# Kernel tuning notes

Measured on AMD Instinct MI355X. Metric: run time of the kernel, lower is better.

The kernel has to match this reference:

```python
import jax, jax.numpy as jnp
import numpy as np

DIM = 768; HEADS = 12; HEAD_DIM = 64; WIN = 14; AC = 192; R = 32; S = 1.0
SCALE = HEAD_DIM ** -0.5
EPS = 1e-5  # torch nn.LayerNorm default


def _ln(x, w, b):
    mu = x.mean(-1, keepdims=True)
    var = ((x - mu) ** 2).mean(-1, keepdims=True)
    return (x - mu) * jax.lax.rsqrt(var + EPS) * w + b


def _rel(rel_pos, n):
    # q_size == k_size == n, rel_pos has 2n-1 rows -> no interpolation branch
    coords = jnp.arange(n)[:, None] - jnp.arange(n)[None, :] + (n - 1)
    return rel_pos[coords]  # [n, n, HEAD_DIM]


def _window_partition(x, ws):
    B, H, W, C = x.shape
    ph = (ws - H % ws) % ws; pw = (ws - W % ws) % ws
    x = jnp.pad(x, ((0, 0), (0, ph), (0, pw), (0, 0)))
    Hp, Wp = H + ph, W + pw
    x = x.reshape(B, Hp // ws, ws, Wp // ws, ws, C).transpose(0, 1, 3, 2, 4, 5)
    return x.reshape(-1, ws, ws, C), (Hp, Wp)


def _window_unpartition(win, ws, pad_hw, hw):
    Hp, Wp = pad_hw; H, W = hw
    B = win.shape[0] // (Hp * Wp // ws // ws)
    x = win.reshape(B, Hp // ws, Wp // ws, ws, ws, -1).transpose(0, 1, 3, 2, 4, 5)
    x = x.reshape(B, Hp, Wp, -1)
    return x[:, :H, :W, :]


def _attention(xw, qkv_W, qkv_b, facu_W, facv_W, qfac_W, vfac_W, rel_h, rel_w, proj_W, proj_b):
    Bw, h, w, _ = xw.shape
    N = h * w
    qkv = xw @ qkv_W.T + qkv_b                     # [Bw, h, w, 3*DIM]
    fu = xw @ facu_W.T                              # FacTu; dropout = identity (eval)
    new_q = (fu @ qfac_W.T) @ facv_W.T              # q_FacTs -> FacTv
    new_v = (fu @ vfac_W.T) @ facv_W.T              # v_FacTs -> FacTv
    qkv = qkv.at[..., :DIM].add(new_q * S)
    qkv = qkv.at[..., 2 * DIM:].add(new_v * S)
    qkv = qkv.reshape(Bw, N, 3, HEADS, HEAD_DIM).transpose(2, 0, 3, 1, 4)
    qkv = qkv.reshape(3, Bw * HEADS, N, HEAD_DIM)
    q, k, v = qkv[0], qkv[1], qkv[2]
    attn = (q * SCALE) @ k.transpose(0, 2, 1)       # [Bw*HEADS, N, N]
    Rh = _rel(rel_h, h); Rw = _rel(rel_w, w)
    r_q = q.reshape(-1, h, w, HEAD_DIM)
    dh = jnp.einsum('bhwc,hkc->bhwk', r_q, Rh)
    dw = jnp.einsum('bhwc,wkc->bhwk', r_q, Rw)
    attn = (attn.reshape(-1, h, w, h, w) + dh[:, :, :, :, None] + dw[:, :, :, None, :]).reshape(-1, N, N)
    attn = jax.nn.softmax(attn, axis=-1)
    out = (attn @ v).reshape(Bw, HEADS, h, w, HEAD_DIM).transpose(0, 2, 3, 1, 4).reshape(Bw, h, w, DIM)
    return out @ proj_W.T + proj_b


def _adapter(x, d_size, nw, nb, dW, db, cW, cb, uW, ub):
    b, h, w, _ = x.shape
    y = _ln(x, nw, nb)
    y = y @ dW.T + db                               # [b, h, w, AC]
    y = y.reshape(b // d_size, d_size, h, w, AC).transpose(0, 4, 1, 2, 3)  # NCDHW
    y = jax.lax.conv_general_dilated(y, cW, (1, 1, 1), 'SAME',
                                     dimension_numbers=('NCDHW', 'OIDHW', 'NCDHW'))
    y = y + cb[None, :, None, None, None]
    y = y.transpose(0, 2, 3, 4, 1).reshape(b, h, w, AC)
    y = jax.nn.gelu(y, approximate=False)
    return x + (y @ uW.T + ub)


def reference(x, an1_w, an1_b, ad1_W, ad1_b, ac1_W, ac1_b, au1_W, au1_b,
              n1_w, n1_b, qkv_W, qkv_b, facu_W, facv_W, qfac_W, vfac_W,
              rel_h, rel_w, proj_W, proj_b,
              an2_w, an2_b, ad2_W, ad2_b, ac2_W, ac2_b, au2_W, au2_b,
              n2_w, n2_b, mlp_W1, mlp_b1, mlp_W2, mlp_b2, d_size):
    x = _adapter(x, d_size, an1_w, an1_b, ad1_W, ad1_b, ac1_W, ac1_b, au1_W, au1_b)
    shortcut = x
    y = _ln(x, n1_w, n1_b)
    H, W = y.shape[1], y.shape[2]
    y, pad_hw = _window_partition(y, WIN)
    y = _attention(y, qkv_W, qkv_b, facu_W, facv_W, qfac_W, vfac_W, rel_h, rel_w, proj_W, proj_b)
    y = _window_unpartition(y, WIN, pad_hw, (H, W))
    x = shortcut + y
    x = _adapter(x, d_size, an2_w, an2_b, ad2_W, ad2_b, ac2_W, ac2_b, au2_W, au2_b)
    h = _ln(x, n2_w, n2_b)
    h = jax.nn.gelu(h @ mlp_W1.T + mlp_b1, approximate=False)
    return x + (h @ mlp_W2.T + mlp_b2)


def setup_inputs() -> dict:
    key = jax.random.key(0)
    ks = iter(jax.random.split(key, 64))
    def rn(shape, scale=0.02):
        return jax.random.normal(next(ks), shape, dtype=jnp.float32) * scale
    B, D, HW = 1, 5, 64
    inp = {'x': jax.random.normal(next(ks), (B * D, HW, HW, DIM), dtype=jnp.float32)}
    for p in ('1', '2'):
        inp[f'an{p}_w'] = jnp.ones((DIM,), jnp.float32)
        inp[f'an{p}_b'] = jnp.zeros((DIM,), jnp.float32)
        inp[f'ad{p}_W'] = rn((AC, DIM)); inp[f'ad{p}_b'] = jnp.zeros((AC,), jnp.float32)
        inp[f'ac{p}_W'] = rn((AC, AC, 3, 3, 3)); inp[f'ac{p}_b'] = jnp.zeros((AC,), jnp.float32)
        inp[f'au{p}_W'] = rn((DIM, AC)); inp[f'au{p}_b'] = jnp.zeros((DIM,), jnp.float32)
    inp['n1_w'] = jnp.ones((DIM,), jnp.float32); inp['n1_b'] = jnp.zeros((DIM,), jnp.float32)
    inp['qkv_W'] = rn((3 * DIM, DIM)); inp['qkv_b'] = jnp.zeros((3 * DIM,), jnp.float32)
    inp['facu_W'] = rn((R, DIM)); inp['facv_W'] = rn((DIM, R))
    inp['qfac_W'] = rn((R, R)); inp['vfac_W'] = rn((R, R))
    inp['rel_h'] = rn((2 * WIN - 1, HEAD_DIM)); inp['rel_w'] = rn((2 * WIN - 1, HEAD_DIM))
    inp['proj_W'] = rn((DIM, DIM)); inp['proj_b'] = jnp.zeros((DIM,), jnp.float32)
    inp['n2_w'] = jnp.ones((DIM,), jnp.float32); inp['n2_b'] = jnp.zeros((DIM,), jnp.float32)
    inp['mlp_W1'] = rn((4 * DIM, DIM)); inp['mlp_b1'] = jnp.zeros((4 * DIM,), jnp.float32)
    inp['mlp_W2'] = rn((DIM, 4 * DIM)); inp['mlp_b2'] = jnp.zeros((DIM,), jnp.float32)
    inp['d_size'] = D
    return inp
```

## Files before the change

### kernel.cpp

```cpp
#include <hip/hip_runtime.h>

typedef unsigned short u16;
typedef __bf16 v8bf __attribute__((ext_vector_type(8)));
typedef unsigned short v8u __attribute__((ext_vector_type(8)));
typedef unsigned short v4u __attribute__((ext_vector_type(4)));
typedef float f32x4 __attribute__((ext_vector_type(4)));
typedef float v8f __attribute__((ext_vector_type(8)));

static constexpr int DIMC = 768;
static constexpr int HEADS = 12;
static constexpr int WINS  = 14;
static constexpr int ACCH  = 192;
static constexpr int NTOK  = 196;
static constexpr int MW    = 24500;
static constexpr int MWP   = 24576;
static constexpr int MS    = 20480;

__device__ __forceinline__ float bf2f(u16 u) {
  union { unsigned int i; float f; } x; x.i = ((unsigned int)u) << 16; return x.f;
}
__device__ __forceinline__ u16 f2bf(float f) {
  union { float f; unsigned int i; } x; x.f = f;
  unsigned int r = x.i + 0x7fffu + ((x.i >> 16) & 1u);
  return (u16)(r >> 16);
}
__device__ __forceinline__ float gelu_f(float x) {
  float y = 0.79788456080286536f * (x + 0.044715f * x * x * x);
  y = fminf(fmaxf(y, -15.f), 15.f);
  const float e = __expf(2.f * y);
  const float th = 1.f - 2.f * __builtin_amdgcn_rcpf(e + 1.f);
  return 0.5f * x * (1.f + th);
}
__device__ __forceinline__ void cp16(const u16* g, u16* l) {
  __builtin_amdgcn_global_load_lds(
      (const __attribute__((address_space(1))) unsigned int*)(const void*)g,
      (__attribute__((address_space(3))) unsigned int*)(void*)l, 16, 0, 0);
}

__global__ void k_zero16(u16* p, int n) {
  int i = blockIdx.x * 256 + threadIdx.x;
  if (i < n) p[i] = 0;
}
__global__ void k_compute_U(const float* __restrict__ facu, const float* __restrict__ qfac,
                            const float* __restrict__ vfac, float* __restrict__ Uq,
                            float* __restrict__ Uv) {
  int idx = blockIdx.x * 256 + threadIdx.x;
  if (idx >= 2 * 768 * 32) return;
  const int which = idx / (768 * 32);
  const int rem = idx - which * 768 * 32;
  const int k = rem >> 5, b = rem & 31;
  const float* fac = which ? vfac : qfac;
  float s = 0.f;
  for (int a = 0; a < 32; ++a) s += facu[a * 768 + k] * fac[b * 32 + a];
  (which ? Uv : Uq)[rem] = s;
}
__global__ void k_build_wcomb(const float* __restrict__ qkvW, const float* __restrict__ Uq,
                              const float* __restrict__ Uv, const float* __restrict__ facv,
                              u16* __restrict__ Wc) {
  int idx = blockIdx.x * 256 + threadIdx.x;
  if (idx >= 2304 * 768) return;
  const int n = idx / 768, k = idx - n * 768;
  float v = qkvW[idx];
  if (n < 768) {
    float s = 0.f;
    for (int b = 0; b < 32; ++b) s += Uq[k * 32 + b] * facv[n * 32 + b];
    v += s;
  } else if (n >= 1536) {
    const int nn = n - 1536;
    float s = 0.f;
    for (int b = 0; b < 32; ++b) s += Uv[k * 32 + b] * facv[nn * 32 + b];
    v += s;
  }
  Wc[idx] = f2bf(v);
}
__global__ void k_cast_pad(const float* __restrict__ src, u16* __restrict__ dst,
                           int rows, int cols, int rowsPad) {
  int idx = blockIdx.x * 256 + threadIdx.x;
  const int base = idx * 4;
  if (base >= rowsPad * cols) return;
  const int r = base / cols;
  v4u o;
  if (r < rows) {
    const float4 v = *(const float4*)(src + base);
    o[0] = f2bf(v.x); o[1] = f2bf(v.y); o[2] = f2bf(v.z); o[3] = f2bf(v.w);
  } else {
    o[0] = o[1] = o[2] = o[3] = 0;
  }
  *(v4u*)(dst + base) = o;
}
__global__ void k_conv_repack(const float* __restrict__ src, u16* __restrict__ dst) {
  int idx = blockIdx.x * 256 + threadIdx.x;
  const int base = idx * 4;
  if (base >= 256 * 5184) return;
  const int co = base / 5184;
  const int rem = base - co * 5184;
  const int tap = rem / 192, ci = rem - tap * 192;
  v4u o;
  if (co < 192) {
    const float* sp = src + co * 5184 + ci * 27 + tap;
#pragma unroll
    for (int e = 0; e < 4; ++e) o[e] = f2bf(sp[e * 27]);
  } else {
    o[0] = o[1] = o[2] = o[3] = 0;
  }
  *(v4u*)(dst + base) = o;
}

template<bool WINDOWED>
__global__ __launch_bounds__(256)
void ln_k(const float* __restrict__ X, const float* __restrict__ w,
          const float* __restrict__ b, u16* __restrict__ out) {
  const int r = (int)blockIdx.x;
  const int t = (int)threadIdx.x;
  int src = r;
  bool zero = false;
  if (WINDOWED) {
    if (r >= MW) zero = true;
    else {
      const int win = r / NTOK, tk = r - win * NTOK;
      const int img = win / 25, wrem = win - img * 25, wy = wrem / 5, wx = wrem - wy * 5;
      const int ty = tk / WINS, tx = tk - ty * WINS;
      const int y = wy * WINS + ty, x = wx * WINS + tx;
      if (y >= 64 || x >= 64) zero = true;
      else src = (img << 12) + (y << 6) + x;
    }
  }
  u16* orow = out + (size_t)r * DIMC;
  if (zero) {
    for (int c = t; c < DIMC; c += 256) orow[c] = 0;
    return;
  }
  const float* xr = X + (size_t)src * DIMC;
  const float v0 = xr[t], v1 = xr[t + 256], v2 = xr[t + 512];
  float s = v0 + v1 + v2, ss = v0 * v0 + v1 * v1 + v2 * v2;
#pragma unroll
  for (int o = 32; o > 0; o >>= 1) { s += __shfl_xor(s, o, 64); ss += __shfl_xor(ss, o, 64); }
  __shared__ float red[8];
  const int wave = t >> 6, lane = t & 63;
  if (lane == 0) { red[wave] = s; red[4 + wave] = ss; }
  __syncthreads();
  s = red[0] + red[1] + red[2] + red[3];
  ss = red[4] + red[5] + red[6] + red[7];
  const float mean = s * (1.0f / 768.0f);
  const float var = ss * (1.0f / 768.0f) - mean * mean;
  const float rstd = rsqrtf(var + 1e-5f);
  orow[t]       = f2bf((v0 - mean) * rstd * w[t]       + b[t]);
  orow[t + 256] = f2bf((v1 - mean) * rstd * w[t + 256] + b[t + 256]);
  orow[t + 512] = f2bf((v2 - mean) * rstd * w[t + 512] + b[t + 512]);
}

template<int EPI, bool CONV>
__global__ __launch_bounds__(256)
void gemm_bt(const u16* __restrict__ A, const u16* __restrict__ B,
             const float* __restrict__ bias, const float* __restrict__ resid,
             float* __restrict__ outF, u16* __restrict__ outB,
             int M, int N, int K, const u16* __restrict__ zrow, int GN) {
  __shared__ u16 smem[2 * 128 * 64];
  u16* At = smem;
  u16* Bt = smem + 128 * 64;
  const int gx = (int)gridDim.x;
  const int nwg = gx * (int)gridDim.y;
  const int lin = (int)blockIdx.y * gx + (int)blockIdx.x;
  const int csz = nwg >> 3;
  const int xcd = lin & 7;
  const int c = lin >> 3;
  const int bmc = csz / gx;
  const int gsz = bmc * GN;
  const int grp = c / gsz, rr = c - grp * gsz;
  const int bn = grp * GN + (rr % GN);
  const int bm = xcd * bmc + (rr / GN);
  const int t = (int)threadIdx.x;
  const int wave = t >> 6, lane = t & 63;
  const int wm = wave >> 1, wn = wave & 1;
  const int lrow = lane >> 3;
  const int c16s = (lane & 7) ^ lrow;
  const int li = lane & 15, lq = lane >> 4;

  f32x4 acc[4][4];
  const f32x4 vzero = {0.f, 0.f, 0.f, 0.f};
#pragma unroll
  for (int a = 0; a < 4; ++a)
#pragma unroll
    for (int b = 0; b < 4; ++b) acc[a][b] = vzero;

  const int nk = K >> 6;
  for (int kt = 0; kt < nk; ++kt) {
    int cD = 0, cY = 0, cX = 0, cblk = 0;
    if (CONV) {
      const int tap = kt / 3;
      cblk = (kt - tap * 3) << 6;
      const int kd = tap / 9, r9 = tap - kd * 9, ky = r9 / 3;
      cD = kd - 1; cY = ky - 1; cX = (r9 - ky * 3) - 1;
    }
#pragma unroll
    for (int i = 0; i < 4; ++i) {
      const int r0 = i * 32 + wave * 8;
      const int grow = bm * 128 + r0 + lrow;
      const u16* src;
      if (CONV) {
        const int d = (grow >> 12) + cD, y = ((grow >> 6) & 63) + cY, x = (grow & 63) + cX;
        if ((unsigned)d < 5u && (unsigned)y < 64u && (unsigned)x < 64u)
          src = A + (size_t)((d << 12) + (y << 6) + x) * ACCH + cblk + c16s * 8;
        else
          src = zrow + c16s * 8;
      } else {
        src = A + (size_t)grow * K + (kt << 6) + c16s * 8;
      }
      cp16(src, &At[r0 * 64]);
    }
#pragma unroll
    for (int i = 0; i < 4; ++i) {
      const int r0 = i * 32 + wave * 8;
      const int grow = bn * 128 + r0 + lrow;
      cp16(B + (size_t)grow * K + (kt << 6) + c16s * 8, &Bt[r0 * 64]);
    }
    __syncthreads();
#pragma unroll
    for (int kk = 0; kk < 2; ++kk) {
      v8bf af[4], bg[4];
#pragma unroll
      for (int mf = 0; mf < 4; ++mf) {
        const int row = wm * 64 + mf * 16 + li;
        const int c16 = (kk * 4 + lq) ^ (li & 7);
        af[mf] = *(const v8bf*)&At[row * 64 + c16 * 8];
      }
#pragma unroll
      for (int nf = 0; nf < 4; ++nf) {
        const int row = wn * 64 + nf * 16 + li;
        const int c16 = (kk * 4 + lq) ^ (li & 7);
        bg[nf] = *(const v8bf*)&Bt[row * 64 + c16 * 8];
      }
#pragma unroll
      for (int mf = 0; mf < 4; ++mf)
#pragma unroll
        for (int nf = 0; nf < 4; ++nf)
          acc[mf][nf] = __builtin_amdgcn_mfma_f32_16x16x32_bf16(af[mf], bg[nf], acc[mf][nf], 0, 0, 0);
    }
    __syncthreads();
  }

  if (EPI == 1 || EPI == 2 || EPI == 4) {
    u16* Ct = smem;
#pragma unroll
    for (int mf = 0; mf < 4; ++mf)
#pragma unroll
      for (int nf = 0; nf < 4; ++nf)
#pragma unroll
        for (int r = 0; r < 4; ++r) {
          const int row = wm * 64 + mf * 16 + lq * 4 + r;
          const int col = wn * 64 + nf * 16 + li;
          float v = acc[mf][nf][r] + bias[bn * 128 + col];
          if (EPI == 2) v = gelu_f(v);
          Ct[row * 128 + (col ^ ((row & 7) << 3))] = f2bf(v);
        }
    __syncthreads();
#pragma unroll
    for (int it = 0; it < 8; ++it) {
      const int row = it * 16 + (t >> 4);
      const int seg = t & 15;
      const int gr = bm * 128 + row;
      const int col8 = bn * 128 + seg * 8;
      if (gr < M && col8 < N) {
        v8u val = *(const v8u*)&Ct[row * 128 + ((seg ^ (row & 7)) * 8)];
        if (EPI == 4) {
          const int sec = col8 / 768;
          const int hm = col8 - sec * 768;
          const int hd = hm >> 6, dd = hm & 63;
          const int win = gr / 196, tk = gr - win * 196;
          *(v8u*)(outB + (size_t)(((win * HEADS + hd) * 3 + sec) * NTOK + tk) * 64 + dd) = val;
        } else {
          *(v8u*)(outB + (size_t)gr * N + col8) = val;
        }
      }
    }
  } else {
    float* Cf = (float*)smem;
#pragma unroll
    for (int h2 = 0; h2 < 2; ++h2) {
      if (h2) __syncthreads();
      if (wm == h2) {
#pragma unroll
        for (int mf = 0; mf < 4; ++mf)
#pragma unroll
          for (int nf = 0; nf < 4; ++nf)
#pragma unroll
            for (int r = 0; r < 4; ++r) {
              const int row = mf * 16 + lq * 4 + r;
              const int col = wn * 64 + nf * 16 + li;
              const float v = acc[mf][nf][r] + bias[bn * 128 + col];
              Cf[row * 128 + (col ^ (((row >> 2) & 3) << 3))] = v;
            }
      }
      __syncthreads();
#pragma unroll
      for (int it = 0; it < 4; ++it) {
        const int row = it * 16 + (t >> 4);
        const int seg = t & 15;
        const int gr = bm * 128 + h2 * 64 + row;
        const int col8 = bn * 128 + seg * 8;
        if (gr < M && col8 < N) {
          v8f val = *(const v8f*)&Cf[row * 128 + ((seg ^ ((row >> 2) & 3)) * 8)];
          if (EPI == 3) {
            const float* rp = resid + (size_t)gr * N + col8;
#pragma unroll
            for (int e = 0; e < 8; ++e) val[e] += rp[e];
            *(v8f*)(outF + (size_t)gr * N + col8) = val;
          } else {
            const int win = gr / 196, tk = gr - win * 196;
            const int img = win / 25, wrem = win - img * 25, wy = wrem / 5, wx = wrem - wy * 5;
            const int ty = tk / WINS, tx = tk - ty * WINS;
            const int y = wy * WINS + ty, x = wx * WINS + tx;
            if (y < 64 && x < 64) {
              const size_t o = (size_t)((img << 12) + (y << 6) + x) * DIMC + col8;
              const float* rp = resid + o;
#pragma unroll
              for (int e = 0; e < 8; ++e) val[e] += rp[e];
              *(v8f*)(outF + o) = val;
            }
          }
        }
      }
    }
  }
}

__global__ __launch_bounds__(512, 2)
void attn_k(const u16* __restrict__ qkvR, const float* __restrict__ relh,
            const float* __restrict__ relw, u16* __restrict__ out) {
  const int blk = (int)blockIdx.x;
  const int win = blk / HEADS, h = blk - win * HEADS;
  const int t = (int)threadIdx.x, w = t >> 6, lane = t & 63;
  const int li = lane & 15, g = lane >> 4;
  const int nmf = (w < 6) ? 2 : (w == 6 ? 1 : 0);

  __shared__ u16 Kt[64 * 64];
  __shared__ u16 Vt[64 * 64];
  __shared__ u16 Pb[8 * 32 * 32];
  __shared__ u16 dhwT[28 * 268];

  const u16* Qb = qkvR + (size_t)(win * HEADS + h) * 3 * NTOK * 64;
  const u16* Kb = Qb + NTOK * 64;
  const u16* Vb = Kb + NTOK * 64;

  v8bf qf[2][2];
#pragma unroll
  for (int mf = 0; mf < 2; ++mf) {
    const int row = min(32 * w + mf * 16 + li, NTOK - 1);
#pragma unroll
    for (int ks = 0; ks < 2; ++ks)
      qf[mf][ks] = *(const v8bf*)(Qb + (size_t)row * 64 + ks * 32 + g * 8);
  }

  u16* relb = Pb;
  for (int idx = t; idx < 2 * 32 * 64; idx += 512) {
    const int which = idx >> 11, rem = idx & 2047, r = rem >> 6, c = rem & 63;
    const float v = (r < 27) ? (which ? relw[r * 64 + c] : relh[r * 64 + c]) : 0.f;
    relb[which * 2048 + r * 64 + (((c >> 3) ^ (r & 7)) * 8) + (c & 7)] = f2bf(v);
  }
  __syncthreads();

  {
    f32x4 dacc[2][2], eacc[2][2];
    const f32x4 vz = {0.f, 0.f, 0.f, 0.f};
#pragma unroll
    for (int mf = 0; mf < 2; ++mf)
#pragma unroll
      for (int nf = 0; nf < 2; ++nf) { dacc[mf][nf] = vz; eacc[mf][nf] = vz; }
#pragma unroll
    for (int ks = 0; ks < 2; ++ks) {
#pragma unroll
      for (int nf = 0; nf < 2; ++nf) {
        const int row = nf * 16 + li;
        const int off = row * 64 + (((ks * 4 + g) ^ (li & 7)) * 8);
        v8bf bh = *(const v8bf*)&relb[off];
        v8bf bw = *(const v8bf*)&relb[2048 + off];
#pragma unroll
        for (int mf = 0; mf < 2; ++mf) if (mf < nmf) {
          dacc[mf][nf] = __builtin_amdgcn_mfma_f32_16x16x32_bf16(qf[mf][ks], bh, dacc[mf][nf], 0, 0, 0);
          eacc[mf][nf] = __builtin_amdgcn_mfma_f32_16x16x32_bf16(qf[mf][ks], bw, eacc[mf][nf], 0, 0, 0);
        }
      }
    }
#pragma unroll
    for (int mf = 0; mf < 2; ++mf) if (mf < nmf)
#pragma unroll
      for (int nf = 0; nf < 2; ++nf)
#pragma unroll
        for (int r = 0; r < 4; ++r) {
          const int i = 32 * w + mf * 16 + 4 * g + r;
          if (i < 196) {
            const int c = nf * 16 + li;
            const int ih = (i * 2341) >> 15, iw = i - ih * 14;
            const int jh = ih + 13 - c;
            if ((unsigned)jh < 14u) dhwT[jh * 268 + i] = f2bf(dacc[mf][nf][r]);
            const int jw = iw + 13 - c;
            if ((unsigned)jw < 14u) dhwT[(14 + jw) * 268 + i] = f2bf(eacc[mf][nf][r]);
          }
        }
  }
  __syncthreads();

  f32x4 oacc[2][4];
  const f32x4 vz = {0.f, 0.f, 0.f, 0.f};
#pragma unroll
  for (int a = 0; a < 2; ++a)
#pragma unroll
    for (int b = 0; b < 4; ++b) oacc[a][b] = vz;
  float mrun[8], lrun[8];
#pragma unroll
  for (int a = 0; a < 8; ++a) { mrun[a] = -1e30f; lrun[a] = 0.f; }

  u16* Pw = Pb + w * 1024;
  const int jv = t & 63;
  const int dv = w * 8;

  for (int jt = 0; jt < 4; ++jt) {
    const int j0 = jt * 64;
    const int njf = (jt < 3) ? 4 : 1;
    const int nhalf = (jt < 3) ? 2 : 1;

    {
      const int rbase = w * 8;
      const int row = rbase + (lane >> 3);
      const int jg = min(j0 + row, NTOK - 1);
      const int cbs = (lane & 7) ^ (row & 7);
      cp16(Kb + (size_t)jg * 64 + cbs * 8, &Kt[rbase * 64]);
    }
    __builtin_amdgcn_sched_barrier(0);
    const int jgv = min(j0 + jv, NTOK - 1);
    v8u vg = *(const v8u*)(Vb + (size_t)jgv * 64 + dv);
    __builtin_amdgcn_sched_barrier(0);
    asm volatile("s_waitcnt vmcnt(1)" ::: "memory");
    __builtin_amdgcn_sched_barrier(0);
    __builtin_amdgcn_s_barrier();
    __builtin_amdgcn_sched_barrier(0);

    f32x4 sacc[2][4];
#pragma unroll
    for (int a = 0; a < 2; ++a)
#pragma unroll
      for (int b = 0; b < 4; ++b) sacc[a][b] = vz;
    if (nmf > 0) {
#pragma unroll
      for (int ks = 0; ks < 2; ++ks) {
#pragma unroll
        for (int jf = 0; jf < 4; ++jf) if (jf < njf) {
          const int row = jf * 16 + li;
          v8bf kb = *(const v8bf*)&Kt[row * 64 + (((ks * 4 + g) ^ (li & 7)) * 8)];
#pragma unroll
          for (int mf = 0; mf < 2; ++mf) if (mf < nmf)
            sacc[mf][jf] = __builtin_amdgcn_mfma_f32_16x16x32_bf16(qf[mf][ks], kb, sacc[mf][jf], 0, 0, 0);
        }
      }
    }

    asm volatile("s_waitcnt vmcnt(0)" ::: "memory");
    __builtin_amdgcn_sched_barrier(0);
#pragma unroll
    for (int e = 0; e < 8; ++e) {
      const int da = dv + e;
      Vt[da * 64 + (((jv >> 3) ^ (da & 7)) * 8) + (jv & 7)] = vg[e];
    }

#pragma unroll
    for (int jf = 0; jf < 4; ++jf) if (jf < njf) {
      const int j = j0 + jf * 16 + li;
      const bool jok = j < 196;
      int jh = (j * 2341) >> 15;
      const int jw = j - jh * 14;
      if (jh > 13) jh = 13;
#pragma unroll
      for (int mf = 0; mf < 2; ++mf) if (mf < nmf) {
        const int i0 = 32 * w + mf * 16 + 4 * g;
        v4u hv = *(const v4u*)&dhwT[jh * 268 + i0];
        v4u wv = *(const v4u*)&dhwT[(14 + jw) * 268 + i0];
#pragma unroll
        for (int r = 0; r < 4; ++r) {
          float v;
          if (jok && (i0 + r) < 196)
            v = sacc[mf][jf][r] * 0.125f + bf2f(hv[r]) + bf2f(wv[r]);
          else v = -1e30f;
          sacc[mf][jf][r] = v;
        }
      }
    }

#pragma unroll
    for (int mf = 0; mf < 2; ++mf) if (mf < nmf)
#pragma unroll
      for (int r = 0; r < 4; ++r) {
        float tmx = -1e30f;
#pragma unroll
        for (int jf = 0; jf < 4; ++jf) if (jf < njf) tmx = fmaxf(tmx, sacc[mf][jf][r]);
#pragma unroll
        for (int o = 1; o < 16; o <<= 1) tmx = fmaxf(tmx, __shfl_xor(tmx, o, 16));
        const int idx = mf * 4 + r;
        const float mnew = fmaxf(mrun[idx], tmx);
        const float sf = __expf(mrun[idx] - mnew);
        mrun[idx] = mnew;
        float ls = 0.f;
#pragma unroll
        for (int jf = 0; jf < 4; ++jf) if (jf < njf) {
          const float p = __expf(sacc[mf][jf][r] - mnew);
          sacc[mf][jf][r] = p;
          ls += p;
        }
#pragma unroll
        for (int o = 1; o < 16; o <<= 1) ls += __shfl_xor(ls, o, 16);
        lrun[idx] = lrun[idx] * sf + ls;
#pragma unroll
        for (int nf = 0; nf < 4; ++nf) oacc[mf][nf][r] *= sf;
      }

#pragma unroll
    for (int half = 0; half < 2; ++half) if (half < nhalf) {
#pragma unroll
      for (int c = 0; c < 2; ++c) {
        const int jf = half * 2 + c;
        const int jloc = c * 16 + li;
#pragma unroll
        for (int mf = 0; mf < 2; ++mf)
#pragma unroll
          for (int r = 0; r < 4; ++r) {
            const int il = mf * 16 + 4 * g + r;
            u16 pv = 0;
            if (mf < nmf && jf < njf) pv = f2bf(sacc[mf][jf][r]);
            Pw[il * 32 + (jloc ^ (g << 3))] = pv;
          }
      }
      if (half == 0) __syncthreads();
      if (nmf > 0) {
        v8bf pa[2];
#pragma unroll
        for (int mf = 0; mf < 2; ++mf) {
          const int row = mf * 16 + li;
          pa[mf] = *(const v8bf*)&Pw[row * 32 + ((g ^ ((li >> 2) & 3)) * 8)];
        }
#pragma unroll
        for (int nf = 0; nf < 4; ++nf) {
          const int d = nf * 16 + li;
          v8bf vb = *(const v8bf*)&Vt[d * 64 + (((half * 4 + g) ^ (li & 7)) * 8)];
#pragma unroll
          for (int mf = 0; mf < 2; ++mf)
            oacc[mf][nf] = __builtin_amdgcn_mfma_f32_16x16x32_bf16(pa[mf], vb, oacc[mf][nf], 0, 0, 0);
        }
      }
    }
    __syncthreads();
  }

  if (nmf > 0) {
    float rinv[8];
#pragma unroll
    for (int a = 0; a < 8; ++a) rinv[a] = 1.0f / lrun[a];
#pragma unroll
    for (int half = 0; half < 2; ++half) {
#pragma unroll
      for (int c = 0; c < 2; ++c) {
        const int nf = half * 2 + c;
        const int dloc = c * 16 + li;
#pragma unroll
        for (int mf = 0; mf < 2; ++mf)
#pragma unroll
          for (int r = 0; r < 4; ++r) {
            const int il = mf * 16 + 4 * g + r;
            float val = (mf < nmf) ? oacc[mf][nf][r] * rinv[mf * 4 + r] : 0.f;
            Pw[il * 32 + (dloc ^ (g << 3))] = f2bf(val);
          }
      }
#pragma unroll
      for (int p = 0; p < 2; ++p) {
        const int row = p * 16 + (lane >> 2);
        const int seg = lane & 3;
        const int i = 32 * w + row;
        if (i < 196) {
          const int segp = seg ^ ((row >> 2) & 3);
          v8u val = *(const v8u*)&Pw[row * 32 + segp * 8];
          *(v8u*)(out + (size_t)(win * NTOK + i) * DIMC + h * 64 + half * 32 + seg * 8) = val;
        }
      }
    }
  }
}

extern "C" void kernel_launch(void* const* d_in, const int* in_sizes, int n_in,
                              void* d_out, int out_size, void* d_ws, size_t ws_size,
                              hipStream_t stream) {
  (void)in_sizes; (void)n_in; (void)out_size; (void)ws_size;
  const float* x0     = (const float*)d_in[0];
  const float* an1_w  = (const float*)d_in[1];
  const float* an1_b  = (const float*)d_in[2];
  const float* ad1_W  = (const float*)d_in[3];
  const float* ad1_b  = (const float*)d_in[4];
  const float* ac1_W  = (const float*)d_in[5];
  const float* ac1_b  = (const float*)d_in[6];
  const float* au1_W  = (const float*)d_in[7];
  const float* au1_b  = (const float*)d_in[8];
  const float* an2_w  = (const float*)d_in[9];
  const float* an2_b  = (const float*)d_in[10];
  const float* ad2_W  = (const float*)d_in[11];
  const float* ad2_b  = (const float*)d_in[12];
  const float* ac2_W  = (const float*)d_in[13];
  const float* ac2_b  = (const float*)d_in[14];
  const float* au2_W  = (const float*)d_in[15];
  const float* au2_b  = (const float*)d_in[16];
  const float* n1_w   = (const float*)d_in[17];
  const float* n1_b   = (const float*)d_in[18];
  const float* qkv_W  = (const float*)d_in[19];
  const float* qkv_b  = (const float*)d_in[20];
  const float* facu_W = (const float*)d_in[21];
  const float* facv_W = (const float*)d_in[22];
  const float* qfac_W = (const float*)d_in[23];
  const float* vfac_W = (const float*)d_in[24];
  const float* rel_h  = (const float*)d_in[25];
  const float* rel_w  = (const float*)d_in[26];
  const float* proj_W = (const float*)d_in[27];
  const float* proj_b = (const float*)d_in[28];
  const float* n2_w   = (const float*)d_in[29];
  const float* n2_b   = (const float*)d_in[30];
  const float* mlp_W1 = (const float*)d_in[31];
  const float* mlp_b1 = (const float*)d_in[32];
  const float* mlp_W2 = (const float*)d_in[33];
  const float* mlp_b2 = (const float*)d_in[34];

  char* ws = (char*)d_ws;
  size_t off = 0;
  auto alloc = [&](size_t bytes) -> void* {
    void* p = (void*)(ws + off);
    off += (bytes + 255) & ~(size_t)255;
    return p;
  };
  u16*  bufA  = (u16*)alloc((size_t)MS * 3072 * 2);
  u16*  bufB  = (u16*)alloc((size_t)MWP * DIMC * 2);
  float* bufX = (float*)alloc((size_t)MS * DIMC * 4);
  u16*  bufD  = (u16*)alloc((size_t)MS * ACCH * 2);
  u16*  bufE  = (u16*)alloc((size_t)MS * ACCH * 2);
  u16*  Wcomb = (u16*)alloc((size_t)2304 * 768 * 2);
  u16*  Wproj = (u16*)alloc((size_t)768 * 768 * 2);
  u16*  Wm1   = (u16*)alloc((size_t)3072 * 768 * 2);
  u16*  Wm2   = (u16*)alloc((size_t)768 * 3072 * 2);
  u16*  Wad1  = (u16*)alloc((size_t)256 * 768 * 2);
  u16*  Wau1  = (u16*)alloc((size_t)768 * 192 * 2);
  u16*  Wcv1  = (u16*)alloc((size_t)256 * 5184 * 2);
  u16*  Wad2  = (u16*)alloc((size_t)256 * 768 * 2);
  u16*  Wau2  = (u16*)alloc((size_t)768 * 192 * 2);
  u16*  Wcv2  = (u16*)alloc((size_t)256 * 5184 * 2);
  float* Uq   = (float*)alloc(768 * 32 * 4);
  float* Uv   = (float*)alloc(768 * 32 * 4);
  u16*  zrow  = (u16*)alloc(256);

  k_zero16<<<1, 256, 0, stream>>>(zrow, 128);
  k_compute_U<<<192, 256, 0, stream>>>(facu_W, qfac_W, vfac_W, Uq, Uv);
  k_build_wcomb<<<(2304 * 768 + 255) / 256, 256, 0, stream>>>(qkv_W, Uq, Uv, facv_W, Wcomb);
  k_cast_pad<<<(768 * 768 / 4 + 255) / 256, 256, 0, stream>>>(proj_W, Wproj, 768, 768, 768);
  k_cast_pad<<<(3072 * 768 / 4 + 255) / 256, 256, 0, stream>>>(mlp_W1, Wm1, 3072, 768, 3072);
  k_cast_pad<<<(768 * 3072 / 4 + 255) / 256, 256, 0, stream>>>(mlp_W2, Wm2, 768, 3072, 768);
  k_cast_pad<<<(256 * 768 / 4 + 255) / 256, 256, 0, stream>>>(ad1_W, Wad1, 192, 768, 256);
  k_cast_pad<<<(768 * 192 / 4 + 255) / 256, 256, 0, stream>>>(au1_W, Wau1, 768, 192, 768);
  k_cast_pad<<<(256 * 768 / 4 + 255) / 256, 256, 0, stream>>>(ad2_W, Wad2, 192, 768, 256);
  k_cast_pad<<<(768 * 192 / 4 + 255) / 256, 256, 0, stream>>>(au2_W, Wau2, 768, 192, 768);
  k_conv_repack<<<(256 * 5184 / 4 + 255) / 256, 256, 0, stream>>>(ac1_W, Wcv1);
  k_conv_repack<<<(256 * 5184 / 4 + 255) / 256, 256, 0, stream>>>(ac2_W, Wcv2);

  ln_k<false><<<MS, 256, 0, stream>>>(x0, an1_w, an1_b, bufB);
  gemm_bt<1, false><<<dim3(2, 160), 256, 0, stream>>>(bufB, Wad1, ad1_b, nullptr, nullptr, bufD, MS, 192, 768, nullptr, 2);
  gemm_bt<2, true><<<dim3(2, 160), 256, 0, stream>>>(bufD, Wcv1, ac1_b, nullptr, nullptr, bufE, MS, 192, 5184, zrow, 2);
  gemm_bt<3, false><<<dim3(6, 160), 256, 0, stream>>>(bufE, Wau1, au1_b, x0, bufX, nullptr, MS, 768, 192, nullptr, 6);

  ln_k<true><<<MWP, 256, 0, stream>>>(bufX, n1_w, n1_b, bufB);
  gemm_bt<4, false><<<dim3(18, 192), 256, 0, stream>>>(bufB, Wcomb, qkv_b, nullptr, nullptr, bufA, MW, 2304, 768, nullptr, 6);
  attn_k<<<125 * HEADS, 512, 0, stream>>>(bufA, rel_h, rel_w, bufB);
  gemm_bt<5, false><<<dim3(6, 192), 256, 0, stream>>>(bufB, Wproj, proj_b, bufX, bufX, nullptr, MW, 768, 768, nullptr, 6);

  ln_k<false><<<MS, 256, 0, stream>>>(bufX, an2_w, an2_b, bufB);
  gemm_bt<1, false><<<dim3(2, 160), 256, 0, stream>>>(bufB, Wad2, ad2_b, nullptr, nullptr, bufD, MS, 192, 768, nullptr, 2);
  gemm_bt<2, true><<<dim3(2, 160), 256, 0, stream>>>(bufD, Wcv2, ac2_b, nullptr, nullptr, bufE, MS, 192, 5184, zrow, 2);
  gemm_bt<3, false><<<dim3(6, 160), 256, 0, stream>>>(bufE, Wau2, au2_b, bufX, bufX, nullptr, MS, 768, 192, nullptr, 6);

  ln_k<false><<<MS, 256, 0, stream>>>(bufX, n2_w, n2_b, bufB);
  gemm_bt<2, false><<<dim3(24, 160), 256, 0, stream>>>(bufB, Wm1, mlp_b1, nullptr, nullptr, bufA, MS, 3072, 768, nullptr, 8);
  gemm_bt<3, false><<<dim3(6, 160), 256, 0, stream>>>(bufA, Wm2, mlp_b2, bufX, (float*)d_out, nullptr, MS, 768, 3072, nullptr, 6);
}
```

Measured before the change: 1.127 ms.

## Add 128x256 wide-tile GEMM with XCD-aware block mapping for large GEMMs

Adds a gemm_wide kernel that uses 128x256 output tiles, with each of the four waves owning a 128x64 slice (8x4 MFMA fragments). It uses a 1D grid whose blocks are remapped so that each XCD handles a contiguous band of M rows, grouped along N for L2 reuse. The up-projection, qkv, proj and MLP GEMMs are routed to it, and the old gemm_bt loses its fp32/EPI4 epilogue paths. The aim is higher arithmetic intensity per LDS load and better cache locality. The cost is more accumulator registers, and the epilogue now runs in chunks with extra barriers.

```diff
diff --git a/kernel.cpp b/kernel.cpp
--- a/kernel.cpp
+++ b/kernel.cpp
@@ -239,67 +239,173 @@
     __syncthreads();
   }
 
-  if (EPI == 1 || EPI == 2 || EPI == 4) {
+  u16* Ct = smem;
+#pragma unroll
+  for (int mf = 0; mf < 4; ++mf)
+#pragma unroll
+    for (int nf = 0; nf < 4; ++nf)
+#pragma unroll
+      for (int r = 0; r < 4; ++r) {
+        const int row = wm * 64 + mf * 16 + lq * 4 + r;
+        const int col = wn * 64 + nf * 16 + li;
+        float v = acc[mf][nf][r] + bias[bn * 128 + col];
+        if (EPI == 2) v = gelu_f(v);
+        Ct[row * 128 + (col ^ ((row & 7) << 3))] = f2bf(v);
+      }
+  __syncthreads();
+#pragma unroll
+  for (int it = 0; it < 8; ++it) {
+    const int row = it * 16 + (t >> 4);
+    const int seg = t & 15;
+    const int gr = bm * 128 + row;
+    const int col8 = bn * 128 + seg * 8;
+    if (gr < M && col8 < N) {
+      v8u val = *(const v8u*)&Ct[row * 128 + ((seg ^ (row & 7)) * 8)];
+      *(v8u*)(outB + (size_t)gr * N + col8) = val;
+    }
+  }
+}
+
+template<int EPI>
+__global__ __launch_bounds__(256)
+void gemm_wide(const u16* __restrict__ A, const u16* __restrict__ B,
+               const float* __restrict__ bias, const float* __restrict__ resid,
+               float* __restrict__ outF, u16* __restrict__ outB,
+               int M, int N, int K, int GN) {
+  __shared__ u16 smem[(128 + 256) * 64];
+  u16* At = smem;
+  u16* Bt = smem + 128 * 64;
+  const int gx = N >> 8;
+  const int nwg = (int)gridDim.x;
+  const int lin = (int)blockIdx.x;
+  const int csz = nwg >> 3;
+  const int xcd = lin & 7;
+  const int c = lin >> 3;
+  const int bmc = csz / gx;
+  const int gsz = bmc * GN;
+  const int grp = c / gsz, rr = c - grp * gsz;
+  const int bn = grp * GN + (rr % GN);
+  const int bm = xcd * bmc + (rr / GN);
+  const int t = (int)threadIdx.x;
+  const int wave = t >> 6, lane = t & 63;
+  const int lrow = lane >> 3;
+  const int c16s = (lane & 7) ^ lrow;
+  const int li = lane & 15, lq = lane >> 4;
+
+  f32x4 acc[8][4];
+  const f32x4 vz = {0.f, 0.f, 0.f, 0.f};
+#pragma unroll
+  for (int a = 0; a < 8; ++a)
+#pragma unroll
+    for (int b = 0; b < 4; ++b) acc[a][b] = vz;
+
+  const u16* Arow = A + (size_t)(bm * 128) * K;
+  const u16* Brow = B + (size_t)(bn * 256) * K;
+
+  const int nk = K >> 6;
+  for (int kt = 0; kt < nk; ++kt) {
+#pragma unroll
+    for (int i = 0; i < 4; ++i) {
+      const int r0 = i * 32 + wave * 8;
+      const int row = r0 + lrow;
+      cp16(Arow + (size_t)row * K + (kt << 6) + c16s * 8, &At[r0 * 64]);
+    }
+#pragma unroll
+    for (int i = 0; i < 8; ++i) {
+      const int r0 = i * 32 + wave * 8;
+      const int row = r0 + lrow;
+      cp16(Brow + (size_t)row * K + (kt << 6) + c16s * 8, &Bt[r0 * 64]);
+    }
+    __syncthreads();
+#pragma unroll
+    for (int kk = 0; kk < 2; ++kk) {
+      const int c16 = (kk * 4 + lq) ^ (li & 7);
+      v8bf af[8], bg[4];
+#pragma unroll
+      for (int mf = 0; mf < 8; ++mf) {
+        const int row = mf * 16 + li;
+        af[mf] = *(const v8bf*)&At[row * 64 + c16 * 8];
+      }
+#pragma unroll
+      for (int nf = 0; nf < 4; ++nf) {
+        const int row = wave * 64 + nf * 16 + li;
+        bg[nf] = *(const v8bf*)&Bt[row * 64 + c16 * 8];
+      }
+#pragma unroll
+      for (int mf = 0; mf < 8; ++mf)
+#pragma unroll
+        for (int nf = 0; nf < 4; ++nf)
+          acc[mf][nf] = __builtin_amdgcn_mfma_f32_16x16x32_bf16(af[mf], bg[nf], acc[mf][nf], 0, 0, 0);
+    }
+    __syncthreads();
+  }
+
+  if (EPI == 2 || EPI == 4) {
     u16* Ct = smem;
 #pragma unroll
-    for (int mf = 0; mf < 4; ++mf)
-#pragma unroll
-      for (int nf = 0; nf < 4; ++nf)
-#pragma unroll
-        for (int r = 0; r < 4; ++r) {
-          const int row = wm * 64 + mf * 16 + lq * 4 + r;
-          const int col = wn * 64 + nf * 16 + li;
-          float v = acc[mf][nf][r] + bias[bn * 128 + col];
-          if (EPI == 2) v = gelu_f(v);
-          Ct[row * 128 + (col ^ ((row & 7) << 3))] = f2bf(v);
-        }
-    __syncthreads();
-#pragma unroll
-    for (int it = 0; it < 8; ++it) {
-      const int row = it * 16 + (t >> 4);
-      const int seg = t & 15;
-      const int gr = bm * 128 + row;
-      const int col8 = bn * 128 + seg * 8;
-      if (gr < M && col8 < N) {
-        v8u val = *(const v8u*)&Ct[row * 128 + ((seg ^ (row & 7)) * 8)];
-        if (EPI == 4) {
-          const int sec = col8 / 768;
-          const int hm = col8 - sec * 768;
-          const int hd = hm >> 6, dd = hm & 63;
-          const int win = gr / 196, tk = gr - win * 196;
-          *(v8u*)(outB + (size_t)(((win * HEADS + hd) * 3 + sec) * NTOK + tk) * 64 + dd) = val;
-        } else {
-          *(v8u*)(outB + (size_t)gr * N + col8) = val;
+    for (int ch = 0; ch < 2; ++ch) {
+      if (ch) __syncthreads();
+#pragma unroll
+      for (int m2 = 0; m2 < 4; ++m2) {
+        const int mf = ch * 4 + m2;
+#pragma unroll
+        for (int nf = 0; nf < 4; ++nf)
+#pragma unroll
+          for (int r = 0; r < 4; ++r) {
+            const int lr = m2 * 16 + lq * 4 + r;
+            const int col = wave * 64 + nf * 16 + li;
+            float v = acc[mf][nf][r] + bias[bn * 256 + col];
+            if (EPI == 2) v = gelu_f(v);
+            Ct[lr * 256 + (col ^ ((lr & 7) << 3))] = f2bf(v);
+          }
+      }
+      __syncthreads();
+#pragma unroll
+      for (int pass = 0; pass < 8; ++pass) {
+        const int row = pass * 8 + (t >> 5);
+        const int seg = t & 31;
+        const int gr = bm * 128 + ch * 64 + row;
+        const int col8 = bn * 256 + seg * 8;
+        if (gr < M) {
+          v8u val = *(const v8u*)&Ct[row * 256 + ((seg ^ (row & 7)) * 8)];
+          if (EPI == 4) {
+            const int sec = col8 / 768;
+            const int hm = col8 - sec * 768;
+            const int hd = hm >> 6, dd = hm & 63;
+            const int win = gr / 196, tk = gr - win * 196;
+            *(v8u*)(outB + (size_t)(((win * HEADS + hd) * 3 + sec) * NTOK + tk) * 64 + dd) = val;
+          } else {
+            *(v8u*)(outB + (size_t)gr * N + col8) = val;
+          }
         }
       }
     }
   } else {
     float* Cf = (float*)smem;
 #pragma unroll
-    for (int h2 = 0; h2 < 2; ++h2) {
-      if (h2) __syncthreads();
-      if (wm == h2) {
-#pragma unroll
-        for (int mf = 0; mf < 4; ++mf)
-#pragma unroll
-          for (int nf = 0; nf < 4; ++nf)
-#pragma unroll
-            for (int r = 0; r < 4; ++r) {
-              const int row = mf * 16 + lq * 4 + r;
-              const int col = wn * 64 + nf * 16 + li;
-              const float v = acc[mf][nf][r] + bias[bn * 128 + col];
-              Cf[row * 128 + (col ^ (((row >> 2) & 3) << 3))] = v;
-            }
+    for (int ch = 0; ch < 4; ++ch) {
+      if (ch) __syncthreads();
+#pragma unroll
+      for (int m2 = 0; m2 < 2; ++m2) {
+        const int mf = ch * 2 + m2;
+#pragma unroll
+        for (int nf = 0; nf < 4; ++nf)
+#pragma unroll
+          for (int r = 0; r < 4; ++r) {
+            const int lr = m2 * 16 + lq * 4 + r;
+            const int col = wave * 64 + nf * 16 + li;
+            Cf[lr * 256 + (col ^ ((lr & 3) << 3))] = acc[mf][nf][r] + bias[bn * 256 + col];
+          }
       }
       __syncthreads();
 #pragma unroll
-      for (int it = 0; it < 4; ++it) {
-        const int row = it * 16 + (t >> 4);
-        const int seg = t & 15;
-        const int gr = bm * 128 + h2 * 64 + row;
-        const int col8 = bn * 128 + seg * 8;
-        if (gr < M && col8 < N) {
-          v8f val = *(const v8f*)&Cf[row * 128 + ((seg ^ ((row >> 2) & 3)) * 8)];
+      for (int pass = 0; pass < 4; ++pass) {
+        const int row = pass * 8 + (t >> 5);
+        const int seg = t & 31;
+        const int gr = bm * 128 + ch * 32 + row;
+        const int col8 = bn * 256 + seg * 8;
+        if (gr < M) {
+          v8f val = *(const v8f*)&Cf[row * 256 + ((seg ^ (row & 3)) * 8)];
           if (EPI == 3) {
             const float* rp = resid + (size_t)gr * N + col8;
 #pragma unroll
@@ -665,19 +771,19 @@
   ln_k<false><<<MS, 256, 0, stream>>>(x0, an1_w, an1_b, bufB);
   gemm_bt<1, false><<<dim3(2, 160), 256, 0, stream>>>(bufB, Wad1, ad1_b, nullptr, nullptr, bufD, MS, 192, 768, nullptr, 2);
   gemm_bt<2, true><<<dim3(2, 160), 256, 0, stream>>>(bufD, Wcv1, ac1_b, nullptr, nullptr, bufE, MS, 192, 5184, zrow, 2);
-  gemm_bt<3, false><<<dim3(6, 160), 256, 0, stream>>>(bufE, Wau1, au1_b, x0, bufX, nullptr, MS, 768, 192, nullptr, 6);
+  gemm_wide<3><<<480, 256, 0, stream>>>(bufE, Wau1, au1_b, x0, bufX, nullptr, MS, 768, 192, 3);
 
   ln_k<true><<<MWP, 256, 0, stream>>>(bufX, n1_w, n1_b, bufB);
-  gemm_bt<4, false><<<dim3(18, 192), 256, 0, stream>>>(bufB, Wcomb, qkv_b, nullptr, nullptr, bufA, MW, 2304, 768, nullptr, 6);
+  gemm_wide<4><<<1728, 256, 0, stream>>>(bufB, Wcomb, qkv_b, nullptr, nullptr, bufA, MW, 2304, 768, 3);
   attn_k<<<125 * HEADS, 512, 0, stream>>>(bufA, rel_h, rel_w, bufB);
-  gemm_bt<5, false><<<dim3(6, 192), 256, 0, stream>>>(bufB, Wproj, proj_b, bufX, bufX, nullptr, MW, 768, 768, nullptr, 6);
+  gemm_wide<5><<<576, 256, 0, stream>>>(bufB, Wproj, proj_b, bufX, bufX, nullptr, MW, 768, 768, 3);
 
   ln_k<false><<<MS, 256, 0, stream>>>(bufX, an2_w, an2_b, bufB);
   gemm_bt<1, false><<<dim3(2, 160), 256, 0, stream>>>(bufB, Wad2, ad2_b, nullptr, nullptr, bufD, MS, 192, 768, nullptr, 2);
   gemm_bt<2, true><<<dim3(2, 160), 256, 0, stream>>>(bufD, Wcv2, ac2_b, nullptr, nullptr, bufE, MS, 192, 5184, zrow, 2);
-  gemm_bt<3, false><<<dim3(6, 160), 256, 0, stream>>>(bufE, Wau2, au2_b, bufX, bufX, nullptr, MS, 768, 192, nullptr, 6);
+  gemm_wide<3><<<480, 256, 0, stream>>>(bufE, Wau2, au2_b, bufX, bufX, nullptr, MS, 768, 192, 3);
 
   ln_k<false><<<MS, 256, 0, stream>>>(bufX, n2_w, n2_b, bufB);
-  gemm_bt<2, false><<<dim3(24, 160), 256, 0, stream>>>(bufB, Wm1, mlp_b1, nullptr, nullptr, bufA, MS, 3072, 768, nullptr, 8);
-  gemm_bt<3, false><<<dim3(6, 160), 256, 0, stream>>>(bufA, Wm2, mlp_b2, bufX, (float*)d_out, nullptr, MS, 768, 3072, nullptr, 6);
-}
+  gemm_wide<2><<<1920, 256, 0, stream>>>(bufB, Wm1, mlp_b1, nullptr, nullptr, bufA, MS, 3072, 768, 4);
+  gemm_wide<3><<<480, 256, 0, stream>>>(bufA, Wm2, mlp_b2, bufX, (float*)d_out, nullptr, MS, 768, 3072, 3);
+}
```

After: 1.344 ms. 19.3% more time.
